# Kernel optimization log

Hardware: AMD Instinct MI355X
Metric: run time of the kernel (lower is better)

Reference implementation:

```python
import jax, jax.numpy as jnp
import numpy as np

N_NODES = 100000
N_EDGES = 1600000
N_CLASS = 10
HIDDEN = 128
BN_EPS = 1e-5


def _bn(h, gamma, beta):
    # BatchNorm1d in training mode: biased batch statistics over the node dim
    m = h.mean(axis=0)
    v = ((h - m) ** 2).mean(axis=0)
    return gamma * (h - m) / jnp.sqrt(v + BN_EPS) + beta


def _mlp(h, w1, b1, g1, t1, w2, b2, g2, t2):
    h = jax.nn.relu(_bn(h @ w1 + b1, g1, t1))
    h = jax.nn.relu(_bn(h @ w2 + b2, g2, t2))
    return h


def _gin_conv(x, edge_index, mlp_params):
    src, dst = edge_index[0], edge_index[1]
    # sum-aggregate neighbor messages: [E, D] gather + scatter-add -> [N, D]
    agg = jax.ops.segment_sum(x[src], dst, num_segments=N_NODES)
    h = x + agg  # (1 + eps) * x + agg, eps = 0
    return _mlp(h, *mlp_params)


def setup_inputs() -> dict:
    key = jax.random.key(0)
    ks = jax.random.split(key, 16)
    x = jax.random.normal(ks[0], (N_NODES, N_CLASS), dtype=jnp.float32)
    edge_index = jax.random.randint(ks[1], (2, N_EDGES), 0, N_NODES, dtype=jnp.int64)
    edge_weight = jax.random.uniform(ks[2], (N_EDGES,), dtype=jnp.float32)

    def lin(k, fan_in, fan_out):
        bound = 1.0 / np.sqrt(fan_in)
        kw, kb = jax.random.split(k)
        w = jax.random.uniform(kw, (fan_in, fan_out), minval=-bound, maxval=bound, dtype=jnp.float32)
        b = jax.random.uniform(kb, (fan_out,), minval=-bound, maxval=bound, dtype=jnp.float32)
        return w, b

    w11, b11 = lin(ks[3], N_CLASS, HIDDEN)
    w12, b12 = lin(ks[4], HIDDEN, HIDDEN)
    w21, b21 = lin(ks[5], HIDDEN, HIDDEN)
    w22, b22 = lin(ks[6], HIDDEN, HIDDEN)
    wf, bf = lin(ks[7], HIDDEN, N_CLASS)
    ones = jnp.ones((HIDDEN,), jnp.float32)
    zeros = jnp.zeros((HIDDEN,), jnp.float32)
    return {
        "x": x, "edge_weight": edge_weight,
        "w11": w11, "b11": b11, "g11": ones, "t11": zeros,
        "w12": w12, "b12": b12, "g12": ones, "t12": zeros,
        "w21": w21, "b21": b21, "g21": ones, "t21": zeros,
        "w22": w22, "b22": b22, "g22": ones, "t22": zeros,
        "wf": wf, "bf": bf,
        "edge_index": edge_index,
    }


def reference(x, edge_weight, w11, b11, g11, t11, w12, b12, g12, t12,
              w21, b21, g21, t21, w22, b22, g22, t22, wf, bf, edge_index):
    h = jax.nn.relu(_gin_conv(x, edge_index, (w11, b11, g11, t11, w12, b12, g12, t12)))
    h = jax.nn.relu(_gin_conv(h, edge_index, (w21, b21, g21, t21, w22, b22, g22, t22)))
    logits = h @ wf + bf
    return jax.nn.log_softmax(logits, axis=1)
```

## Files before the change

### kernel.cpp

```cpp
#include <hip/hip_runtime.h>

#define N_CLASS 10
#define HIDDEN 128
#define BN_EPS 1e-5f

typedef short short8 __attribute__((ext_vector_type(8)));
typedef float floatx4 __attribute__((ext_vector_type(4)));

__device__ __forceinline__ float bf2f(unsigned short u) {
    unsigned int x = ((unsigned int)u) << 16;
    float f; __builtin_memcpy(&f, &x, 4); return f;
}
__device__ __forceinline__ unsigned short f2bf(float f) {
    unsigned int x; __builtin_memcpy(&x, &f, 4);
    x += 0x7FFFu + ((x >> 16) & 1u);
    return (unsigned short)(x >> 16);
}
__device__ __forceinline__ float lo_f(unsigned int u) {
    unsigned int x = u << 16; float f; __builtin_memcpy(&f, &x, 4); return f;
}
__device__ __forceinline__ float hi_f(unsigned int u) {
    unsigned int x = u & 0xffff0000u; float f; __builtin_memcpy(&f, &x, 4); return f;
}

__global__ void hist_k(const int* __restrict__ ei, int* __restrict__ cnt,
                       int* __restrict__ rank, int E) {
    int e = blockIdx.x * 256 + threadIdx.x;
    if (e < E) rank[e] = atomicAdd(cnt + ei[E + e], 1);
}

__global__ void scanA_k(const int* __restrict__ cnt, int* __restrict__ bsum, int N) {
    __shared__ int sm[256];
    int i = blockIdx.x * 256 + threadIdx.x;
    sm[threadIdx.x] = (i < N) ? cnt[i] : 0;
    __syncthreads();
    for (int s = 128; s > 0; s >>= 1) {
        if (threadIdx.x < s) sm[threadIdx.x] += sm[threadIdx.x + s];
        __syncthreads();
    }
    if (threadIdx.x == 0) bsum[blockIdx.x] = sm[0];
}

__global__ void scanB_k(int* __restrict__ bsum, int B) {
    __shared__ int sm[512];
    int t = threadIdx.x;
    sm[t] = (t < B) ? bsum[t] : 0;
    __syncthreads();
    for (int off = 1; off < 512; off <<= 1) {
        int u = (t >= off) ? sm[t - off] : 0;
        __syncthreads();
        sm[t] += u;
        __syncthreads();
    }
    if (t < B) bsum[t] = (t == 0) ? 0 : sm[t - 1];
}

__global__ void scanC_k(const int* __restrict__ cnt, const int* __restrict__ boff,
                        int* __restrict__ row_ptr, int N) {
    __shared__ int sm[256];
    int i = blockIdx.x * 256 + threadIdx.x;
    int t = threadIdx.x;
    int v = (i < N) ? cnt[i] : 0;
    sm[t] = v;
    __syncthreads();
    for (int off = 1; off < 256; off <<= 1) {
        int u = (t >= off) ? sm[t - off] : 0;
        __syncthreads();
        sm[t] += u;
        __syncthreads();
    }
    if (i < N) row_ptr[i] = boff[blockIdx.x] + sm[t] - v;
}

__global__ void fill_k(const int* __restrict__ ei, const int* __restrict__ rank,
                       const int* __restrict__ rp, int* __restrict__ col,
                       int E, int N) {
    const int P = 4;
    const int rs = (N + P - 1) / P;
    const int stride = gridDim.x * 256;
#pragma unroll 1
    for (int pass = 0; pass < P; ++pass) {
        int lo = pass * rs, hi = lo + rs;
        for (int e = blockIdx.x * 256 + threadIdx.x; e < E; e += stride) {
            int d = ei[E + e];
            if (d >= lo && d < hi)
                col[rp[d] + rank[e]] = ei[e];
        }
    }
}

__global__ void prepw_k(const float* __restrict__ W0, const float* __restrict__ W1,
                        const float* __restrict__ W2,
                        unsigned short* __restrict__ T0, unsigned short* __restrict__ T1,
                        unsigned short* __restrict__ T2) {
    const float* W = (blockIdx.y == 0) ? W0 : (blockIdx.y == 1) ? W1 : W2;
    unsigned short* T = (blockIdx.y == 0) ? T0 : (blockIdx.y == 1) ? T1 : T2;
    int i = blockIdx.x * 256 + threadIdx.x;
    if (i < 128 * 128) {
        int k = i >> 7, n = i & 127;
        T[n * 128 + k] = f2bf(W[k * 128 + n]);
    }
}

__global__ void gather10_k(const float* __restrict__ X, const int* __restrict__ col,
                           const int* __restrict__ rp, const int* __restrict__ cnt,
                           float* __restrict__ out, int N) {
    int t = blockIdx.x * 256 + threadIdx.x;
    int node = t / N_CLASS, f = t - node * N_CLASS;
    if (node >= N) return;
    int start = rp[node], deg = cnt[node];
    float acc = X[(size_t)node * N_CLASS + f];
    int j = 0;
    for (; j + 8 <= deg; j += 8) {
        int s0 = col[start + j],     s1 = col[start + j + 1];
        int s2 = col[start + j + 2], s3 = col[start + j + 3];
        int s4 = col[start + j + 4], s5 = col[start + j + 5];
        int s6 = col[start + j + 6], s7 = col[start + j + 7];
        float v0 = X[(size_t)s0 * N_CLASS + f];
        float v1 = X[(size_t)s1 * N_CLASS + f];
        float v2 = X[(size_t)s2 * N_CLASS + f];
        float v3 = X[(size_t)s3 * N_CLASS + f];
        float v4 = X[(size_t)s4 * N_CLASS + f];
        float v5 = X[(size_t)s5 * N_CLASS + f];
        float v6 = X[(size_t)s6 * N_CLASS + f];
        float v7 = X[(size_t)s7 * N_CLASS + f];
        acc += v0; acc += v1; acc += v2; acc += v3;
        acc += v4; acc += v5; acc += v6; acc += v7;
    }
    for (; j < deg; ++j)
        acc += X[(size_t)col[start + j] * N_CLASS + f];
    out[(size_t)node * N_CLASS + f] = acc;
}

__global__ __launch_bounds__(256) void act2_k(
    const unsigned short* __restrict__ Z, unsigned short* __restrict__ R,
    const float* __restrict__ st, const float* __restrict__ g,
    const float* __restrict__ b, int N, float inv_n) {
    __shared__ float sTab[128], hTab[128];
    int tid = threadIdx.x;
    if (tid < 128) {
        float m = st[tid] * inv_n;
        float v = fmaxf(st[128 + tid] * inv_n - m * m, 0.f);
        float s = g[tid] * rsqrtf(v + BN_EPS);
        sTab[tid] = s;
        hTab[tid] = b[tid] - m * s;
    }
    __syncthreads();
    int total = N * 16;
    for (int i = blockIdx.x * 256 + tid; i < total; i += gridDim.x * 256) {
        int k8 = (i & 15) * 8;
        uint4 v = ((const uint4*)Z)[i];
        unsigned short* us = (unsigned short*)&v;
#pragma unroll
        for (int j = 0; j < 8; ++j) {
            float f = fmaxf(fmaf(bf2f(us[j]), sTab[k8 + j], hTab[k8 + j]), 0.f);
            us[j] = f2bf(f);
        }
        ((uint4*)R)[i] = v;
    }
}

__global__ __launch_bounds__(256) void gather_sum_k(
    const unsigned short* __restrict__ R, const int* __restrict__ col,
    const int* __restrict__ rp, const int* __restrict__ cnt,
    unsigned short* __restrict__ out, int N) {
    int wave = (blockIdx.x * 256 + threadIdx.x) >> 6;
    int lane = threadIdx.x & 63;
    if (wave >= N) return;
    int start = rp[wave], deg = cnt[wave];
    const unsigned int* Xv = (const unsigned int*)R;
    unsigned int self = Xv[(size_t)wave * 64 + lane];
    float a0 = lo_f(self);
    float a1 = hi_f(self);
    int j = 0;
    for (; j + 8 <= deg; j += 8) {
        int n0 = col[start + j],     n1 = col[start + j + 1];
        int n2 = col[start + j + 2], n3 = col[start + j + 3];
        int n4 = col[start + j + 4], n5 = col[start + j + 5];
        int n6 = col[start + j + 6], n7 = col[start + j + 7];
        unsigned int w0 = Xv[(size_t)n0 * 64 + lane];
        unsigned int w1 = Xv[(size_t)n1 * 64 + lane];
        unsigned int w2 = Xv[(size_t)n2 * 64 + lane];
        unsigned int w3 = Xv[(size_t)n3 * 64 + lane];
        unsigned int w4 = Xv[(size_t)n4 * 64 + lane];
        unsigned int w5 = Xv[(size_t)n5 * 64 + lane];
        unsigned int w6 = Xv[(size_t)n6 * 64 + lane];
        unsigned int w7 = Xv[(size_t)n7 * 64 + lane];
        a0 += lo_f(w0); a1 += hi_f(w0);
        a0 += lo_f(w1); a1 += hi_f(w1);
        a0 += lo_f(w2); a1 += hi_f(w2);
        a0 += lo_f(w3); a1 += hi_f(w3);
        a0 += lo_f(w4); a1 += hi_f(w4);
        a0 += lo_f(w5); a1 += hi_f(w5);
        a0 += lo_f(w6); a1 += hi_f(w6);
        a0 += lo_f(w7); a1 += hi_f(w7);
    }
    for (; j < deg; ++j) {
        unsigned int v = Xv[(size_t)col[start + j] * 64 + lane];
        a0 += lo_f(v); a1 += hi_f(v);
    }
    unsigned int o = (unsigned int)f2bf(a0) | ((unsigned int)f2bf(a1) << 16);
    ((unsigned int*)out)[(size_t)wave * 64 + lane] = o;
}

__global__ __launch_bounds__(128) void gemm10_k(
    const float* __restrict__ A, const float* __restrict__ W,
    const float* __restrict__ bias, unsigned short* __restrict__ C,
    float* __restrict__ stOut, int N) {
    __shared__ float rb[16 * N_CLASS];
    const int tid = threadIdx.x;
    float wreg[N_CLASS];
#pragma unroll
    for (int k = 0; k < N_CLASS; ++k) wreg[k] = W[k * HIDDEN + tid];
    float bb = bias[tid];
    float s = 0.f, s2 = 0.f;
    for (int r0 = blockIdx.x * 16; r0 < N; r0 += gridDim.x * 16) {
        int nr = min(16, N - r0);
        for (int i = tid; i < nr * N_CLASS; i += 128) rb[i] = A[r0 * N_CLASS + i];
        __syncthreads();
        for (int r = 0; r < nr; ++r) {
            float acc = bb;
#pragma unroll
            for (int k = 0; k < N_CLASS; ++k) acc = fmaf(rb[r * N_CLASS + k], wreg[k], acc);
            C[(size_t)(r0 + r) * HIDDEN + tid] = f2bf(acc);
            s += acc; s2 += acc * acc;
        }
        __syncthreads();
    }
    atomicAdd(stOut + tid, s);
    atomicAdd(stOut + HIDDEN + tid, s2);
}

template<bool BN>
__global__ __launch_bounds__(256) void gemm_mfma_k(
    const unsigned short* __restrict__ Zin, const unsigned short* __restrict__ Wt,
    const float* __restrict__ bias,
    const float* __restrict__ stIn, const float* __restrict__ gIn,
    const float* __restrict__ tIn,
    unsigned short* __restrict__ Zout, float* __restrict__ stOut,
    int N, float inv_n) {
    __shared__ unsigned short Wl[128 * 136];
    __shared__ unsigned short Al[64 * 136];
    __shared__ float sTab[128], hTab[128], biasTab[128];
    __shared__ float redS[128], redS2[128];

    const int tid  = threadIdx.x;
    const int wv   = tid >> 6;
    const int ln   = tid & 63;
    const int half = ln >> 4;
    const int l16  = ln & 15;

    if (tid < 128) {
        biasTab[tid] = bias[tid];
        if (BN) {
            float m = stIn[tid] * inv_n;
            float v = fmaxf(stIn[128 + tid] * inv_n - m * m, 0.f);
            float s = gIn[tid] * rsqrtf(v + BN_EPS);
            sTab[tid] = s;
            hTab[tid] = tIn[tid] - m * s;
        }
        redS[tid] = 0.f; redS2[tid] = 0.f;
    }
    for (int c = tid; c < 2048; c += 256) {
        int n = c >> 4, k8 = c & 15;
        uint4 v = *(const uint4*)(Wt + (size_t)n * 128 + k8 * 8);
        *(uint4*)(&Wl[n * 136 + k8 * 8]) = v;
    }
    __syncthreads();

    float cs[8], cs2[8];
#pragma unroll
    for (int i = 0; i < 8; ++i) { cs[i] = 0.f; cs2[i] = 0.f; }

    const int ntiles = (N + 63) >> 6;
    for (int tile = blockIdx.x; tile < ntiles; tile += gridDim.x) {
        const int r0 = tile * 64;
        for (int c = tid; c < 1024; c += 256) {
            int r = c >> 4, k8 = c & 15;
            int gr = r0 + r; if (gr >= N) gr = N - 1;
            uint4 v = *(const uint4*)(Zin + (size_t)gr * 128 + k8 * 8);
            if (BN) {
                unsigned short* us = (unsigned short*)&v;
                int kb = k8 * 8;
#pragma unroll
                for (int j = 0; j < 8; ++j) {
                    float f = fmaxf(fmaf(bf2f(us[j]), sTab[kb + j], hTab[kb + j]), 0.f);
                    us[j] = f2bf(f);
                }
            }
            *(uint4*)(&Al[r * 136 + k8 * 8]) = v;
        }
        __syncthreads();

        short8 afrag[4];
        const int arow = wv * 16 + l16;
#pragma unroll
        for (int s = 0; s < 4; ++s)
            afrag[s] = *(const short8*)(&Al[arow * 136 + s * 32 + half * 8]);
        __syncthreads();

#pragma unroll
        for (int ct = 0; ct < 8; ++ct) {
            floatx4 acc = {0.f, 0.f, 0.f, 0.f};
            const int bn_ = ct * 16 + l16;
#pragma unroll
            for (int s = 0; s < 4; ++s) {
                short8 bfrag = *(const short8*)(&Wl[bn_ * 136 + s * 32 + half * 8]);
                acc = __builtin_amdgcn_mfma_f32_16x16x32_bf16(afrag[s], bfrag, acc, 0, 0, 0);
            }
            float bcol = biasTab[bn_];
#pragma unroll
            for (int r = 0; r < 4; ++r) {
                int lrow = wv * 16 + half * 4 + r;
                float val = acc[r] + bcol;
                if (r0 + lrow < N) { cs[ct] += val; cs2[ct] += val * val; }
                Al[lrow * 136 + bn_] = f2bf(val);
            }
        }
        __syncthreads();

        for (int c = tid; c < 1024; c += 256) {
            int r = c >> 4, k8 = c & 15;
            int gr = r0 + r;
            if (gr < N)
                *(uint4*)(Zout + (size_t)gr * 128 + k8 * 8) = *(const uint4*)(&Al[r * 136 + k8 * 8]);
        }
        __syncthreads();
    }

#pragma unroll
    for (int ct = 0; ct < 8; ++ct) {
        float a = cs[ct], b = cs2[ct];
        a += __shfl_xor(a, 16); a += __shfl_xor(a, 32);
        b += __shfl_xor(b, 16); b += __shfl_xor(b, 32);
        if (half == 0) {
            atomicAdd(&redS[ct * 16 + l16], a);
            atomicAdd(&redS2[ct * 16 + l16], b);
        }
    }
    __syncthreads();
    if (tid < 128) {
        atomicAdd(stOut + tid, redS[tid]);
        atomicAdd(stOut + 128 + tid, redS2[tid]);
    }
}

__global__ __launch_bounds__(256) void final_mfma_k(
    const unsigned short* __restrict__ Z, const float* __restrict__ st,
    const float* __restrict__ g, const float* __restrict__ b,
    const float* __restrict__ wf, const float* __restrict__ bfc,
    float* __restrict__ out, int N, float inv_n) {
    __shared__ unsigned short Al[64 * 136];
    __shared__ unsigned short Bl[16 * 136];
    __shared__ float sTab[128], hTab[128], biasTab[16];

    const int tid  = threadIdx.x;
    const int wv   = tid >> 6;
    const int ln   = tid & 63;
    const int half = ln >> 4;
    const int l16  = ln & 15;

    if (tid < 128) {
        float m = st[tid] * inv_n;
        float v = fmaxf(st[128 + tid] * inv_n - m * m, 0.f);
        float s = g[tid] * rsqrtf(v + BN_EPS);
        sTab[tid] = s;
        hTab[tid] = b[tid] - m * s;
    }
    if (tid < 16) biasTab[tid] = (tid < N_CLASS) ? bfc[tid] : -3.0e38f;
    {
        int n = tid >> 4, k8 = (tid & 15) * 8;
        uint4 v;
        unsigned short* us = (unsigned short*)&v;
#pragma unroll
        for (int j = 0; j < 8; ++j)
            us[j] = (n < N_CLASS) ? f2bf(wf[(k8 + j) * N_CLASS + n]) : (unsigned short)0;
        *(uint4*)(&Bl[n * 136 + k8]) = v;
    }
    __syncthreads();

    short8 bfrag[4];
#pragma unroll
    for (int s = 0; s < 4; ++s)
        bfrag[s] = *(const short8*)(&Bl[l16 * 136 + s * 32 + half * 8]);

    const int ntiles = (N + 63) >> 6;
    for (int tile = blockIdx.x; tile < ntiles; tile += gridDim.x) {
        const int r0 = tile * 64;
        for (int c = tid; c < 1024; c += 256) {
            int r = c >> 4, k8 = c & 15;
            int gr = r0 + r; if (gr >= N) gr = N - 1;
            uint4 v = *(const uint4*)(Z + (size_t)gr * 128 + k8 * 8);
            unsigned short* us = (unsigned short*)&v;
            int kb = k8 * 8;
#pragma unroll
            for (int j = 0; j < 8; ++j) {
                float f = fmaxf(fmaf(bf2f(us[j]), sTab[kb + j], hTab[kb + j]), 0.f);
                us[j] = f2bf(f);
            }
            *(uint4*)(&Al[r * 136 + k8 * 8]) = v;
        }
        __syncthreads();

        short8 afrag[4];
        const int arow = wv * 16 + l16;
#pragma unroll
        for (int s = 0; s < 4; ++s)
            afrag[s] = *(const short8*)(&Al[arow * 136 + s * 32 + half * 8]);
        __syncthreads();

        floatx4 acc = {0.f, 0.f, 0.f, 0.f};
#pragma unroll
        for (int s = 0; s < 4; ++s)
            acc = __builtin_amdgcn_mfma_f32_16x16x32_bf16(afrag[s], bfrag[s], acc, 0, 0, 0);

        float bcol = biasTab[l16];
#pragma unroll
        for (int r = 0; r < 4; ++r) {
            float lg = acc[r] + bcol;
            float mx = lg;
            mx = fmaxf(mx, __shfl_xor(mx, 1));
            mx = fmaxf(mx, __shfl_xor(mx, 2));
            mx = fmaxf(mx, __shfl_xor(mx, 4));
            mx = fmaxf(mx, __shfl_xor(mx, 8));
            float p = __expf(lg - mx);
            float se = p;
            se += __shfl_xor(se, 1);
            se += __shfl_xor(se, 2);
            se += __shfl_xor(se, 4);
            se += __shfl_xor(se, 8);
            float ls = __logf(se);
            int grow = r0 + wv * 16 + half * 4 + r;
            if (l16 < N_CLASS && grow < N)
                out[(size_t)grow * N_CLASS + l16] = lg - mx - ls;
        }
    }
}


extern "C" void kernel_launch(void* const* d_in, const int* in_sizes, int n_in,
                              void* d_out, int out_size, void* d_ws, size_t ws_size,
                              hipStream_t stream) {
    const float* x   = (const float*)d_in[0];
    const float* w11 = (const float*)d_in[2];
    const float* b11 = (const float*)d_in[3];
    const float* g11 = (const float*)d_in[4];
    const float* t11 = (const float*)d_in[5];
    const float* w12 = (const float*)d_in[6];
    const float* b12 = (const float*)d_in[7];
    const float* g12 = (const float*)d_in[8];
    const float* t12 = (const float*)d_in[9];
    const float* w21 = (const float*)d_in[10];
    const float* b21 = (const float*)d_in[11];
    const float* g21 = (const float*)d_in[12];
    const float* t21 = (const float*)d_in[13];
    const float* w22 = (const float*)d_in[14];
    const float* b22 = (const float*)d_in[15];
    const float* g22 = (const float*)d_in[16];
    const float* t22 = (const float*)d_in[17];
    const float* wf  = (const float*)d_in[18];
    const float* bf  = (const float*)d_in[19];
    const int*   ei  = (const int*)d_in[20];

    const int N = in_sizes[0] / N_CLASS;
    const int E = in_sizes[1];
    const float inv_n = 1.0f / (float)N;

    char* base = (char*)d_ws;
    size_t off = 0;
    auto take = [&](size_t bytes) { void* p = base + off; off += (bytes + 15) & ~(size_t)15; return p; };
    float*          stats   = (float*)take(1024 * 4);
    float*          h0      = (float*)take((size_t)N * N_CLASS * 4);
    int*            cnt     = (int*)take((size_t)N * 4);
    int*            row_ptr = (int*)take((size_t)N * 4);
    int*            rank    = (int*)take((size_t)E * 4);
    int*            bsum    = (int*)take(512 * 4);
    int*            col     = (int*)take((size_t)E * 4);
    unsigned short* bufA    = (unsigned short*)take((size_t)N * HIDDEN * 2);
    unsigned short* bufB    = (unsigned short*)take((size_t)N * HIDDEN * 2);
    unsigned short* bufC    = (unsigned short*)take((size_t)N * HIDDEN * 2);
    unsigned short* Wt1     = (unsigned short*)take(128 * 128 * 2);
    unsigned short* Wt2     = (unsigned short*)take(128 * 128 * 2);
    unsigned short* Wt3     = (unsigned short*)take(128 * 128 * 2);

    const int nB = (N + 255) / 256;
    const int gE = (E + 255) / 256;

    (void)hipMemsetAsync(stats, 0, 1024 * sizeof(float), stream);
    (void)hipMemsetAsync(cnt, 0, (size_t)N * sizeof(int), stream);

    prepw_k<<<dim3(64, 3), 256, 0, stream>>>(w12, w21, w22, Wt1, Wt2, Wt3);

    hist_k<<<gE, 256, 0, stream>>>(ei, cnt, rank, E);
    scanA_k<<<nB, 256, 0, stream>>>(cnt, bsum, N);
    scanB_k<<<1, 512, 0, stream>>>(bsum, nB);
    scanC_k<<<nB, 256, 0, stream>>>(cnt, bsum, row_ptr, N);
    fill_k<<<gE, 256, 0, stream>>>(ei, rank, row_ptr, col, E, N);

    gather10_k<<<(N * N_CLASS + 255) / 256, 256, 0, stream>>>(x, col, row_ptr, cnt, h0, N);
    gemm10_k<<<512, 128, 0, stream>>>(h0, w11, b11, bufA, stats, N);
    gemm_mfma_k<true><<<512, 256, 0, stream>>>(bufA, Wt1, b12, stats, g11, t11,
                                               bufB, stats + 256, N, inv_n);

    act2_k<<<3125, 256, 0, stream>>>(bufB, bufC, stats + 256, g12, t12, N, inv_n);
    gather_sum_k<<<(N * 64 + 255) / 256, 256, 0, stream>>>(bufC, col, row_ptr, cnt,
                                                           bufA, N);

    gemm_mfma_k<false><<<512, 256, 0, stream>>>(bufA, Wt2, b21, nullptr, nullptr, nullptr,
                                                bufB, stats + 512, N, inv_n);
    gemm_mfma_k<true><<<512, 256, 0, stream>>>(bufB, Wt3, b22, stats + 512, g21, t21,
                                               bufA, stats + 768, N, inv_n);

    final_mfma_k<<<782, 256, 0, stream>>>(bufA, stats + 768, g22, t22,
                                          wf, bf, (float*)d_out, N, inv_n);
}
```

Measured before the change: 439.8 us.

## Pad input features to 16, fold memsets into prep kernel, scalarize gather indices

Input features are padded from 10 to 16 floats per node so the first-layer gather uses shift/mask indexing and 64-byte aligned rows, with gemm10 reading the padded layout. The two memsets are folded into the weight-prep kernel, replacing them with in-kernel zeroing. The gather_sum kernel uses readfirstlane to keep node index, row start and degree in scalar registers. Many size_t casts become 32-bit index arithmetic. The changes add an extra pad kernel, extra memory traffic for the padding, and rely on 32-bit index math not overflowing.

```diff
diff --git a/kernel.cpp b/kernel.cpp
--- a/kernel.cpp
+++ b/kernel.cpp
@@ -89,10 +89,11 @@
     }
 }
 
-__global__ void prepw_k(const float* __restrict__ W0, const float* __restrict__ W1,
-                        const float* __restrict__ W2,
-                        unsigned short* __restrict__ T0, unsigned short* __restrict__ T1,
-                        unsigned short* __restrict__ T2) {
+__global__ void prep_k(const float* __restrict__ W0, const float* __restrict__ W1,
+                       const float* __restrict__ W2,
+                       unsigned short* __restrict__ T0, unsigned short* __restrict__ T1,
+                       unsigned short* __restrict__ T2,
+                       float* __restrict__ stats, int* __restrict__ cnt, int N) {
     const float* W = (blockIdx.y == 0) ? W0 : (blockIdx.y == 1) ? W1 : W2;
     unsigned short* T = (blockIdx.y == 0) ? T0 : (blockIdx.y == 1) ? T1 : T2;
     int i = blockIdx.x * 256 + threadIdx.x;
@@ -100,36 +101,47 @@
         int k = i >> 7, n = i & 127;
         T[n * 128 + k] = f2bf(W[k * 128 + n]);
     }
-}
-
-__global__ void gather10_k(const float* __restrict__ X, const int* __restrict__ col,
+    if (blockIdx.y == 0) {
+        if (i < 1024) stats[i] = 0.f;
+        for (int c = i; c < N; c += 64 * 256) cnt[c] = 0;
+    }
+}
+
+__global__ void padx_k(const float* __restrict__ X, float* __restrict__ XP, int N) {
+    int i = blockIdx.x * 256 + threadIdx.x;
+    if (i >= N * 16) return;
+    int node = i >> 4, f = i & 15;
+    XP[i] = (f < N_CLASS) ? X[node * N_CLASS + f] : 0.f;
+}
+
+__global__ void gather10_k(const float* __restrict__ XP, const int* __restrict__ col,
                            const int* __restrict__ rp, const int* __restrict__ cnt,
                            float* __restrict__ out, int N) {
     int t = blockIdx.x * 256 + threadIdx.x;
-    int node = t / N_CLASS, f = t - node * N_CLASS;
+    int node = t >> 4, f = t & 15;
     if (node >= N) return;
     int start = rp[node], deg = cnt[node];
-    float acc = X[(size_t)node * N_CLASS + f];
+    float acc = XP[node * 16 + f];
     int j = 0;
     for (; j + 8 <= deg; j += 8) {
         int s0 = col[start + j],     s1 = col[start + j + 1];
         int s2 = col[start + j + 2], s3 = col[start + j + 3];
         int s4 = col[start + j + 4], s5 = col[start + j + 5];
         int s6 = col[start + j + 6], s7 = col[start + j + 7];
-        float v0 = X[(size_t)s0 * N_CLASS + f];
-        float v1 = X[(size_t)s1 * N_CLASS + f];
-        float v2 = X[(size_t)s2 * N_CLASS + f];
-        float v3 = X[(size_t)s3 * N_CLASS + f];
-        float v4 = X[(size_t)s4 * N_CLASS + f];
-        float v5 = X[(size_t)s5 * N_CLASS + f];
-        float v6 = X[(size_t)s6 * N_CLASS + f];
-        float v7 = X[(size_t)s7 * N_CLASS + f];
+        float v0 = XP[s0 * 16 + f];
+        float v1 = XP[s1 * 16 + f];
+        float v2 = XP[s2 * 16 + f];
+        float v3 = XP[s3 * 16 + f];
+        float v4 = XP[s4 * 16 + f];
+        float v5 = XP[s5 * 16 + f];
+        float v6 = XP[s6 * 16 + f];
+        float v7 = XP[s7 * 16 + f];
         acc += v0; acc += v1; acc += v2; acc += v3;
         acc += v4; acc += v5; acc += v6; acc += v7;
     }
     for (; j < deg; ++j)
-        acc += X[(size_t)col[start + j] * N_CLASS + f];
-    out[(size_t)node * N_CLASS + f] = acc;
+        acc += XP[col[start + j] * 16 + f];
+    out[node * 16 + f] = acc;
 }
 
 __global__ __launch_bounds__(256) void act2_k(
@@ -164,12 +176,13 @@
     const unsigned short* __restrict__ R, const int* __restrict__ col,
     const int* __restrict__ rp, const int* __restrict__ cnt,
     unsigned short* __restrict__ out, int N) {
-    int wave = (blockIdx.x * 256 + threadIdx.x) >> 6;
+    int wave = __builtin_amdgcn_readfirstlane((blockIdx.x * 256 + threadIdx.x) >> 6);
     int lane = threadIdx.x & 63;
     if (wave >= N) return;
-    int start = rp[wave], deg = cnt[wave];
+    int start = __builtin_amdgcn_readfirstlane(rp[wave]);
+    int deg   = __builtin_amdgcn_readfirstlane(cnt[wave]);
     const unsigned int* Xv = (const unsigned int*)R;
-    unsigned int self = Xv[(size_t)wave * 64 + lane];
+    unsigned int self = Xv[wave * 64 + lane];
     float a0 = lo_f(self);
     float a1 = hi_f(self);
     int j = 0;
@@ -178,14 +191,14 @@
         int n2 = col[start + j + 2], n3 = col[start + j + 3];
         int n4 = col[start + j + 4], n5 = col[start + j + 5];
         int n6 = col[start + j + 6], n7 = col[start + j + 7];
-        unsigned int w0 = Xv[(size_t)n0 * 64 + lane];
-        unsigned int w1 = Xv[(size_t)n1 * 64 + lane];
-        unsigned int w2 = Xv[(size_t)n2 * 64 + lane];
-        unsigned int w3 = Xv[(size_t)n3 * 64 + lane];
-        unsigned int w4 = Xv[(size_t)n4 * 64 + lane];
-        unsigned int w5 = Xv[(size_t)n5 * 64 + lane];
-        unsigned int w6 = Xv[(size_t)n6 * 64 + lane];
-        unsigned int w7 = Xv[(size_t)n7 * 64 + lane];
+        unsigned int w0 = Xv[n0 * 64 + lane];
+        unsigned int w1 = Xv[n1 * 64 + lane];
+        unsigned int w2 = Xv[n2 * 64 + lane];
+        unsigned int w3 = Xv[n3 * 64 + lane];
+        unsigned int w4 = Xv[n4 * 64 + lane];
+        unsigned int w5 = Xv[n5 * 64 + lane];
+        unsigned int w6 = Xv[n6 * 64 + lane];
+        unsigned int w7 = Xv[n7 * 64 + lane];
         a0 += lo_f(w0); a1 += hi_f(w0);
         a0 += lo_f(w1); a1 += hi_f(w1);
         a0 += lo_f(w2); a1 += hi_f(w2);
@@ -196,18 +209,18 @@
         a0 += lo_f(w7); a1 += hi_f(w7);
     }
     for (; j < deg; ++j) {
-        unsigned int v = Xv[(size_t)col[start + j] * 64 + lane];
+        unsigned int v = Xv[col[start + j] * 64 + lane];
         a0 += lo_f(v); a1 += hi_f(v);
     }
     unsigned int o = (unsigned int)f2bf(a0) | ((unsigned int)f2bf(a1) << 16);
-    ((unsigned int*)out)[(size_t)wave * 64 + lane] = o;
+    ((unsigned int*)out)[wave * 64 + lane] = o;
 }
 
 __global__ __launch_bounds__(128) void gemm10_k(
     const float* __restrict__ A, const float* __restrict__ W,
     const float* __restrict__ bias, unsigned short* __restrict__ C,
     float* __restrict__ stOut, int N) {
-    __shared__ float rb[16 * N_CLASS];
+    __shared__ float rb[16 * 16];
     const int tid = threadIdx.x;
     float wreg[N_CLASS];
 #pragma unroll
@@ -216,13 +229,13 @@
     float s = 0.f, s2 = 0.f;
     for (int r0 = blockIdx.x * 16; r0 < N; r0 += gridDim.x * 16) {
         int nr = min(16, N - r0);
-        for (int i = tid; i < nr * N_CLASS; i += 128) rb[i] = A[r0 * N_CLASS + i];
+        for (int i = tid; i < nr * 16; i += 128) rb[i] = A[r0 * 16 + i];
         __syncthreads();
         for (int r = 0; r < nr; ++r) {
             float acc = bb;
 #pragma unroll
-            for (int k = 0; k < N_CLASS; ++k) acc = fmaf(rb[r * N_CLASS + k], wreg[k], acc);
-            C[(size_t)(r0 + r) * HIDDEN + tid] = f2bf(acc);
+            for (int k = 0; k < N_CLASS; ++k) acc = fmaf(rb[r * 16 + k], wreg[k], acc);
+            C[(r0 + r) * HIDDEN + tid] = f2bf(acc);
             s += acc; s2 += acc * acc;
         }
         __syncthreads();
@@ -263,7 +276,7 @@
     }
     for (int c = tid; c < 2048; c += 256) {
         int n = c >> 4, k8 = c & 15;
-        uint4 v = *(const uint4*)(Wt + (size_t)n * 128 + k8 * 8);
+        uint4 v = *(const uint4*)(Wt + n * 128 + k8 * 8);
         *(uint4*)(&Wl[n * 136 + k8 * 8]) = v;
     }
     __syncthreads();
@@ -278,7 +291,7 @@
         for (int c = tid; c < 1024; c += 256) {
             int r = c >> 4, k8 = c & 15;
             int gr = r0 + r; if (gr >= N) gr = N - 1;
-            uint4 v = *(const uint4*)(Zin + (size_t)gr * 128 + k8 * 8);
+            uint4 v = *(const uint4*)(Zin + gr * 128 + k8 * 8);
             if (BN) {
                 unsigned short* us = (unsigned short*)&v;
                 int kb = k8 * 8;
@@ -323,7 +336,7 @@
             int r = c >> 4, k8 = c & 15;
             int gr = r0 + r;
             if (gr < N)
-                *(uint4*)(Zout + (size_t)gr * 128 + k8 * 8) = *(const uint4*)(&Al[r * 136 + k8 * 8]);
+                *(uint4*)(Zout + gr * 128 + k8 * 8) = *(const uint4*)(&Al[r * 136 + k8 * 8]);
         }
         __syncthreads();
     }
@@ -390,7 +403,7 @@
         for (int c = tid; c < 1024; c += 256) {
             int r = c >> 4, k8 = c & 15;
             int gr = r0 + r; if (gr >= N) gr = N - 1;
-            uint4 v = *(const uint4*)(Z + (size_t)gr * 128 + k8 * 8);
+            uint4 v = *(const uint4*)(Z + gr * 128 + k8 * 8);
             unsigned short* us = (unsigned short*)&v;
             int kb = k8 * 8;
 #pragma unroll
@@ -432,7 +445,7 @@
             float ls = __logf(se);
             int grow = r0 + wv * 16 + half * 4 + r;
             if (l16 < N_CLASS && grow < N)
-                out[(size_t)grow * N_CLASS + l16] = lg - mx - ls;
+                out[grow * N_CLASS + l16] = lg - mx - ls;
         }
     }
 }
@@ -470,7 +483,8 @@
     size_t off = 0;
     auto take = [&](size_t bytes) { void* p = base + off; off += (bytes + 15) & ~(size_t)15; return p; };
     float*          stats   = (float*)take(1024 * 4);
-    float*          h0      = (float*)take((size_t)N * N_CLASS * 4);
+    float*          xp      = (float*)take((size_t)N * 16 * 4);
+    float*          h0      = (float*)take((size_t)N * 16 * 4);
     int*            cnt     = (int*)take((size_t)N * 4);
     int*            row_ptr = (int*)take((size_t)N * 4);
     int*            rank    = (int*)take((size_t)E * 4);
@@ -486,10 +500,9 @@
     const int nB = (N + 255) / 256;
     const int gE = (E + 255) / 256;
 
-    (void)hipMemsetAsync(stats, 0, 1024 * sizeof(float), stream);
-    (void)hipMemsetAsync(cnt, 0, (size_t)N * sizeof(int), stream);
-
-    prepw_k<<<dim3(64, 3), 256, 0, stream>>>(w12, w21, w22, Wt1, Wt2, Wt3);
+    prep_k<<<dim3(64, 3), 256, 0, stream>>>(w12, w21, w22, Wt1, Wt2, Wt3,
+                                            stats, cnt, N);
+    padx_k<<<(N * 16 + 255) / 256, 256, 0, stream>>>(x, xp, N);
 
     hist_k<<<gE, 256, 0, stream>>>(ei, cnt, rank, E);
     scanA_k<<<nB, 256, 0, stream>>>(cnt, bsum, N);
@@ -497,7 +510,7 @@
     scanC_k<<<nB, 256, 0, stream>>>(cnt, bsum, row_ptr, N);
     fill_k<<<gE, 256, 0, stream>>>(ei, rank, row_ptr, col, E, N);
 
-    gather10_k<<<(N * N_CLASS + 255) / 256, 256, 0, stream>>>(x, col, row_ptr, cnt, h0, N);
+    gather10_k<<<(N * 16 + 255) / 256, 256, 0, stream>>>(xp, col, row_ptr, cnt, h0, N);
     gemm10_k<<<512, 128, 0, stream>>>(h0, w11, b11, bufA, stats, N);
     gemm_mfma_k<true><<<512, 256, 0, stream>>>(bufA, Wt1, b12, stats, g11, t11,
                                                bufB, stats + 256, N, inv_n);
```

Result: no change. 434.9 us (-1.1%).
